# Performance work log

Measured on AMD Instinct MI355X. Metric: run time of the kernel, lower is better.

Reference implementation:

```python
import jax, jax.numpy as jnp
import numpy as np

E, H, V, KV, B, L = 512, 1024, 50257, 1000, 64, 512


def setup_inputs() -> dict:
    key = jax.random.key(0)
    ks = jax.random.split(key, 32)

    def p(i, shape, scale=0.02):
        return jax.random.normal(ks[i], shape, jnp.float32) * scale

    return {
        # forward args
        "input_ids": jax.random.randint(ks[0], (B,), 0, V),
        "h": p(1, (B, H), 1.0),
        "c": p(2, (B, H), 1.0),
        "k": p(3, (KV, E), 1.0),
        "context_vector": p(4, (B, H), 1.0),
        "encoder_outputs": p(5, (B, L, H), 1.0),
        # parameters (stored [in, out])
        "embedding": p(6, (V, E)),
        "W_ih": p(7, (E, 4 * H)),
        "W_hh": p(8, (H, 4 * H)),
        "b_ih": jnp.zeros((4 * H,), jnp.float32),
        "b_hh": jnp.zeros((4 * H,), jnp.float32),
        # attn MLP: Linear(2H,E) Tanh Linear(E,E) Tanh Linear(E,1)
        "aW1": p(9, (2 * H, E)), "ab1": jnp.zeros((E,), jnp.float32),
        "aW2": p(10, (E, E)), "ab2": jnp.zeros((E,), jnp.float32),
        "aW3": p(11, (E, 1)), "ab3": jnp.zeros((1,), jnp.float32),
        # attn_key MLP: Linear(E+2H,E) Tanh Linear(E,E) Tanh Linear(E,1)
        "kW1": p(12, (E + 2 * H, E)), "kb1": jnp.zeros((E,), jnp.float32),
        "kW2": p(13, (E, E)), "kb2": jnp.zeros((E,), jnp.float32),
        "kW3": p(14, (E, 1)), "kb3": jnp.zeros((1,), jnp.float32),
        # attn_linear: Linear(2H, V)
        "alW": p(15, (2 * H, V)), "alb": jnp.zeros((V,), jnp.float32),
    }


def reference(input_ids, h, c, k, context_vector, encoder_outputs,
              embedding, W_ih, W_hh, b_ih, b_hh,
              aW1, ab1, aW2, ab2, aW3, ab3,
              kW1, kb1, kW2, kb2, kW3, kb3,
              alW, alb):
    b = h.shape[0]
    kv = k.shape[0]
    v = alb.shape[0]

    # embedding lookup (dropout is identity in eval)
    x = embedding[input_ids]                                    # [B,E]

    # LSTMCell (PyTorch gate order: i, f, g, o)
    gates = x @ W_ih + h @ W_hh + b_ih + b_hh                   # [B,4H]
    i_g, f_g, g_g, o_g = jnp.split(gates, 4, axis=1)
    c_t = jax.nn.sigmoid(f_g) * c + jax.nn.sigmoid(i_g) * jnp.tanh(g_g)
    h_t = jax.nn.sigmoid(o_g) * jnp.tanh(c_t)                   # [B,H]

    # additive attention over encoder outputs
    h_ext = jnp.broadcast_to(h_t[:, None, :], encoder_outputs.shape)
    u = jnp.concatenate([encoder_outputs, h_ext], axis=2)       # [B,L,2H]
    u = jnp.tanh(u @ aW1 + ab1)
    u = jnp.tanh(u @ aW2 + ab2)
    u = (u @ aW3 + ab3)[..., 0]                                  # [B,L]
    a_t = jax.nn.softmax(u, axis=1)
    h_ctx = jnp.einsum('bl,blh->bh', a_t, encoder_outputs)       # [B,H]

    # key attention: cat(context, h_t, k) -> MLP -> [B,KV]
    ctx_ext = jnp.broadcast_to(context_vector[:, None, :], (b, kv, context_vector.shape[1]))
    ht_ext = jnp.broadcast_to(h_t[:, None, :], (b, kv, h_t.shape[1]))
    k_ext = jnp.broadcast_to(k[None, :, :], (b, kv, k.shape[1]))
    uk = jnp.concatenate([ctx_ext, ht_ext, k_ext], axis=2)       # [B,KV,E+2H]
    uk = jnp.tanh(uk @ kW1 + kb1)
    uk = jnp.tanh(uk @ kW2 + kb2)
    uk = (uk @ kW3 + kb3)[..., 0]                                # [B,KV]

    # zero-pad key logits into the full vocab (first V-KV entries are zero)
    v_k_t = jnp.concatenate([jnp.zeros((b, v - kv), h_t.dtype), uk], axis=1)

    # key_flag == 'True' path
    o_t = jnp.concatenate([h_t, h_ctx], axis=1) @ alW + alb + v_k_t  # [B,V]
    y_t = jax.nn.log_softmax(o_t, axis=1)
    return (y_t, h_t, c_t)
```

## Files before the change

### kernel.cpp

```cpp
#include <hip/hip_runtime.h>
#include <hip/hip_bf16.h>
#include <math.h>

#define EE 512
#define HH 1024
#define VV 50257
#define KVN 1000
#define BB 64
#define LL 512
#define FH 4096
#define TWOH 2048

typedef __hip_bfloat16 bf16;
typedef short bf16x8 __attribute__((ext_vector_type(8)));
typedef float f32x4  __attribute__((ext_vector_type(4)));

__device__ __forceinline__ float sigm(float x){ return 1.0f/(1.0f+__expf(-x)); }

__device__ __forceinline__ unsigned short f2bf(float f){
  unsigned int u = __float_as_uint(f);
  unsigned int r = (u + 0x7FFFu + ((u >> 16) & 1u)) >> 16;
  return (unsigned short)r;
}

__global__ __launch_bounds__(256)
void k_gates_init(const float* __restrict__ b_ih, const float* __restrict__ b_hh,
                  float* __restrict__ gates){
  int i = blockIdx.x*256 + threadIdx.x;
  int j = i & (FH-1);
  gates[i] = b_ih[j] + b_hh[j];
}

__global__ __launch_bounds__(256)
void k_embed_gates(const int* __restrict__ ids, const float* __restrict__ h,
                   const float* __restrict__ emb,
                   const float* __restrict__ W_ih, const float* __restrict__ W_hh,
                   float* __restrict__ gates){
  __shared__ float Xs[64][68];
  __shared__ float Ws[64][68];
  const int tid = threadIdx.x;
  const int nbase = blockIdx.x*64;
  const int kbase = blockIdx.y*64;
  {
    int b = tid >> 2;
    int kof = (tid & 3)*16;
    int id = ids[b];
    #pragma unroll
    for (int i=0;i<16;i++){
      int kg = kbase + kof + i;
      float v = (kg < EE) ? emb[(size_t)id*EE + kg] : h[(size_t)b*HH + (kg-EE)];
      Xs[kof+i][b] = v;
    }
  }
  {
    int n = tid & 63;
    int kr0 = tid >> 6;
    #pragma unroll
    for (int i=0;i<16;i++){
      int kr = kr0 + i*4;
      int kg = kbase + kr;
      float v = (kg < EE) ? W_ih[(size_t)kg*FH + nbase + n]
                          : W_hh[(size_t)(kg-EE)*FH + nbase + n];
      Ws[kr][n] = v;
    }
  }
  __syncthreads();
  const int tx = tid & 15, ty = tid >> 4;
  float acc[4][4] = {};
  for (int k=0;k<64;k++){
    float4 a4 = *(const float4*)(&Xs[k][ty*4]);
    float4 w4 = *(const float4*)(&Ws[k][tx*4]);
    float aa[4] = {a4.x,a4.y,a4.z,a4.w};
    float ww[4] = {w4.x,w4.y,w4.z,w4.w};
    #pragma unroll
    for (int i=0;i<4;i++)
      #pragma unroll
      for (int j=0;j<4;j++)
        acc[i][j] += aa[i]*ww[j];
  }
  #pragma unroll
  for (int i=0;i<4;i++){
    int b = ty*4 + i;
    #pragma unroll
    for (int j=0;j<4;j++)
      atomicAdd(&gates[(size_t)b*FH + nbase + tx*4 + j], acc[i][j]);
  }
}

__global__ __launch_bounds__(256)
void k_lstm(const float* __restrict__ gates, const float* __restrict__ c_in,
            float* __restrict__ hout, float* __restrict__ cout){
  int idx = blockIdx.x*256 + threadIdx.x;
  int b = idx >> 10, hh = idx & 1023;
  const float* g = gates + (size_t)b*FH;
  float ig = g[hh], fg = g[HH+hh], gg = g[2*HH+hh], og = g[3*HH+hh];
  float ct = sigm(fg)*c_in[idx] + sigm(ig)*tanhf(gg);
  float ht = sigm(og)*tanhf(ct);
  hout[idx] = ht;
  cout[idx] = ct;
}

__global__ __launch_bounds__(256)
void k_q1p1(const float* __restrict__ ht, const float* __restrict__ ctx,
            const float* __restrict__ aW1, const float* __restrict__ ab1,
            const float* __restrict__ kW1, const float* __restrict__ kb1,
            float* __restrict__ q1, float* __restrict__ p1){
  int e = blockIdx.x*256 + threadIdx.x;
  int b = blockIdx.y;
  float aq = 0.f, ap = 0.f;
  for (int k2 = 0; k2 < HH; ++k2){
    float hv = ht[(size_t)b*HH + k2];
    float cv = ctx[(size_t)b*HH + k2];
    aq += hv * aW1[(size_t)(HH+k2)*EE + e];
    ap += cv * kW1[(size_t)k2*EE + e];
    ap += hv * kW1[(size_t)(HH+k2)*EE + e];
  }
  q1[(size_t)b*EE + e] = aq + ab1[e];
  p1[(size_t)b*EE + e] = ap + kb1[e];
}

__global__ __launch_bounds__(256)
void k_p2(const float* __restrict__ kin, const float* __restrict__ kW1,
          float* __restrict__ p2){
  int e  = blockIdx.x*256 + threadIdx.x;
  int kv = blockIdx.y;
  float a = 0.f;
  for (int k2 = 0; k2 < EE; ++k2)
    a += kin[(size_t)kv*EE + k2] * kW1[(size_t)(TWOH+k2)*EE + e];
  p2[(size_t)kv*EE + e] = a;
}

__global__ __launch_bounds__(256)
void k_transpose_bf16(const float* __restrict__ W, bf16* __restrict__ Wt,
                      int K, int N){
  __shared__ float t[32][33];
  int k0 = blockIdx.y*32, n0 = blockIdx.x*32;
  int tx = threadIdx.x & 31, ty = threadIdx.x >> 5;
  #pragma unroll
  for (int i=0;i<4;i++){
    int kk = ty + i*8;
    t[kk][tx] = W[(size_t)(k0+kk)*N + n0 + tx];
  }
  __syncthreads();
  #pragma unroll
  for (int i=0;i<4;i++){
    int nn = ty + i*8;
    Wt[(size_t)(n0+nn)*K + k0 + tx] = __float2bfloat16(t[tx][nn]);
  }
}

__global__ __launch_bounds__(256)
void k_mfma_tanh_dot(const bf16* __restrict__ A, const bf16* __restrict__ Wt,
                     const float* __restrict__ bias, const float* __restrict__ w3,
                     float* __restrict__ logits){
  __shared__ short As[128*40];
  __shared__ short Bs[128*40];
  const int tid  = threadIdx.x;
  const int lane = tid & 63, wid = tid >> 6;
  const int wm = wid >> 1, wn = wid & 1;
  const int quad = lane >> 4, l16 = lane & 15;
  const int m0 = blockIdx.y*128, n0 = blockIdx.x*128;

  f32x4 acc[4][4] = {};
  for (int k0 = 0; k0 < 512; k0 += 32){
    #pragma unroll
    for (int it = 0; it < 2; ++it){
      int task = tid + it*256;
      int row = task >> 2, cg = task & 3;
      *(bf16x8*)(As + row*40 + cg*8) =
        *(const bf16x8*)((const short*)A + (size_t)(m0+row)*512 + k0 + cg*8);
      *(bf16x8*)(Bs + row*40 + cg*8) =
        *(const bf16x8*)((const short*)Wt + (size_t)(n0+row)*512 + k0 + cg*8);
    }
    __syncthreads();
    bf16x8 af[4], bfr[4];
    #pragma unroll
    for (int mt=0; mt<4; ++mt)
      af[mt] = *(const bf16x8*)(As + (wm*64 + mt*16 + l16)*40 + quad*8);
    #pragma unroll
    for (int nt=0; nt<4; ++nt)
      bfr[nt] = *(const bf16x8*)(Bs + (wn*64 + nt*16 + l16)*40 + quad*8);
    #pragma unroll
    for (int mt=0; mt<4; ++mt)
      #pragma unroll
      for (int nt=0; nt<4; ++nt)
        acc[mt][nt] = __builtin_amdgcn_mfma_f32_16x16x32_bf16(af[mt], bfr[nt], acc[mt][nt], 0, 0, 0);
    __syncthreads();
  }
  float bv[4], wv[4];
  #pragma unroll
  for (int nt=0; nt<4; ++nt){
    int n = n0 + wn*64 + nt*16 + l16;
    bv[nt] = bias[n]; wv[nt] = w3[n];
  }
  #pragma unroll
  for (int mt=0; mt<4; ++mt){
    #pragma unroll
    for (int r=0; r<4; ++r){
      float s = 0.f;
      #pragma unroll
      for (int nt=0; nt<4; ++nt)
        s += tanhf(acc[mt][nt][r] + bv[nt]) * wv[nt];
      #pragma unroll
      for (int off=8; off>=1; off>>=1) s += __shfl_xor(s, off, 16);
      if (l16 == 0){
        int row = wm*64 + mt*16 + quad*4 + r;
        atomicAdd(&logits[m0 + row], s);
      }
    }
  }
}

__global__ __launch_bounds__(256)
void k_mfma_key(const float* __restrict__ p1, const float* __restrict__ p2,
                const bf16* __restrict__ Wt,
                const float* __restrict__ bias, const float* __restrict__ w3,
                float* __restrict__ logits){
  __shared__ short As[128*40];
  __shared__ short Bs[128*40];
  const int tid  = threadIdx.x;
  const int lane = tid & 63, wid = tid >> 6;
  const int wm = wid >> 1, wn = wid & 1;
  const int quad = lane >> 4, l16 = lane & 15;
  const int m0 = blockIdx.y*128, n0 = blockIdx.x*128;

  f32x4 acc[4][4] = {};
  for (int k0 = 0; k0 < 512; k0 += 32){
    #pragma unroll
    for (int it = 0; it < 2; ++it){
      int grp = tid + it*256;
      int row = grp >> 2, cg = grp & 3;
      int r = m0 + row;
      int b = r / KVN;
      int kv = r - b*KVN;
      int e = k0 + cg*8;
      float4 a0 = *(const float4*)(p1 + (size_t)b*EE + e);
      float4 a1 = *(const float4*)(p1 + (size_t)b*EE + e + 4);
      float4 c0 = *(const float4*)(p2 + (size_t)kv*EE + e);
      float4 c1 = *(const float4*)(p2 + (size_t)kv*EE + e + 4);
      bf16x8 v;
      v[0]=(short)f2bf(tanhf(a0.x+c0.x)); v[1]=(short)f2bf(tanhf(a0.y+c0.y));
      v[2]=(short)f2bf(tanhf(a0.z+c0.z)); v[3]=(short)f2bf(tanhf(a0.w+c0.w));
      v[4]=(short)f2bf(tanhf(a1.x+c1.x)); v[5]=(short)f2bf(tanhf(a1.y+c1.y));
      v[6]=(short)f2bf(tanhf(a1.z+c1.z)); v[7]=(short)f2bf(tanhf(a1.w+c1.w));
      *(bf16x8*)(As + row*40 + cg*8) = v;
      *(bf16x8*)(Bs + row*40 + cg*8) =
        *(const bf16x8*)((const short*)Wt + (size_t)(n0+row)*512 + k0 + cg*8);
    }
    __syncthreads();
    bf16x8 af[4], bfr[4];
    #pragma unroll
    for (int mt=0; mt<4; ++mt)
      af[mt] = *(const bf16x8*)(As + (wm*64 + mt*16 + l16)*40 + quad*8);
    #pragma unroll
    for (int nt=0; nt<4; ++nt)
      bfr[nt] = *(const bf16x8*)(Bs + (wn*64 + nt*16 + l16)*40 + quad*8);
    #pragma unroll
    for (int mt=0; mt<4; ++mt)
      #pragma unroll
      for (int nt=0; nt<4; ++nt)
        acc[mt][nt] = __builtin_amdgcn_mfma_f32_16x16x32_bf16(af[mt], bfr[nt], acc[mt][nt], 0, 0, 0);
    __syncthreads();
  }
  float bv[4], wv[4];
  #pragma unroll
  for (int nt=0; nt<4; ++nt){
    int n = n0 + wn*64 + nt*16 + l16;
    bv[nt] = bias[n]; wv[nt] = w3[n];
  }
  #pragma unroll
  for (int mt=0; mt<4; ++mt){
    #pragma unroll
    for (int r=0; r<4; ++r){
      float s = 0.f;
      #pragma unroll
      for (int nt=0; nt<4; ++nt)
        s += tanhf(acc[mt][nt][r] + bv[nt]) * wv[nt];
      #pragma unroll
      for (int off=8; off>=1; off>>=1) s += __shfl_xor(s, off, 16);
      if (l16 == 0){
        int row = wm*64 + mt*16 + quad*4 + r;
        atomicAdd(&logits[m0 + row], s);
      }
    }
  }
}

__global__ __launch_bounds__(256)
void k_mfma_a1(const float* __restrict__ enc, const bf16* __restrict__ Wt,
               const float* __restrict__ q1, bf16* __restrict__ U1){
  __shared__ short As[128*40];
  __shared__ short Bs[128*40];
  const int tid  = threadIdx.x;
  const int lane = tid & 63, wid = tid >> 6;
  const int wm = wid >> 1, wn = wid & 1;
  const int quad = lane >> 4, l16 = lane & 15;
  const int m0 = blockIdx.y*128, n0 = blockIdx.x*128;

  f32x4 acc[4][4] = {};
  for (int k0 = 0; k0 < 1024; k0 += 32){
    #pragma unroll
    for (int it = 0; it < 4; ++it){
      int task = tid + it*256;
      int row = task >> 3, g = task & 7;
      float4 f = *(const float4*)(enc + (size_t)(m0+row)*1024 + k0 + g*4);
      uint2 pk;
      pk.x = (unsigned int)f2bf(f.x) | ((unsigned int)f2bf(f.y) << 16);
      pk.y = (unsigned int)f2bf(f.z) | ((unsigned int)f2bf(f.w) << 16);
      *(uint2*)(As + row*40 + g*4) = pk;
    }
    #pragma unroll
    for (int it = 0; it < 2; ++it){
      int task = tid + it*256;
      int row = task >> 2, cg = task & 3;
      *(bf16x8*)(Bs + row*40 + cg*8) =
        *(const bf16x8*)((const short*)Wt + (size_t)(n0+row)*1024 + k0 + cg*8);
    }
    __syncthreads();
    bf16x8 af[4], bfr[4];
    #pragma unroll
    for (int mt=0; mt<4; ++mt)
      af[mt] = *(const bf16x8*)(As + (wm*64 + mt*16 + l16)*40 + quad*8);
    #pragma unroll
    for (int nt=0; nt<4; ++nt)
      bfr[nt] = *(const bf16x8*)(Bs + (wn*64 + nt*16 + l16)*40 + quad*8);
    #pragma unroll
    for (int mt=0; mt<4; ++mt)
      #pragma unroll
      for (int nt=0; nt<4; ++nt)
        acc[mt][nt] = __builtin_amdgcn_mfma_f32_16x16x32_bf16(af[mt], bfr[nt], acc[mt][nt], 0, 0, 0);
    __syncthreads();
  }
  const int b = m0 >> 9;
  const float* q1r = q1 + (size_t)b*EE;
  #pragma unroll
  for (int mt=0; mt<4; ++mt){
    #pragma unroll
    for (int r=0; r<4; ++r){
      int m = m0 + wm*64 + mt*16 + quad*4 + r;
      #pragma unroll
      for (int nt=0; nt<4; ++nt){
        int n = n0 + wn*64 + nt*16 + l16;
        U1[(size_t)m*EE + n] = __float2bfloat16(tanhf(acc[mt][nt][r] + q1r[n]));
      }
    }
  }
}

__global__ __launch_bounds__(256)
void k_init_logits(float* __restrict__ ulog, float* __restrict__ uklog,
                   const float* __restrict__ ab3, const float* __restrict__ kb3){
  int i = blockIdx.x*256 + threadIdx.x;
  if (i < BB*LL)  ulog[i]  = ab3[0];
  if (i < BB*KVN) uklog[i] = kb3[0];
}

__global__ __launch_bounds__(256)
void k_softmax(float* __restrict__ ulog){
  __shared__ float sdata[256];
  int b = blockIdx.x, tid = threadIdx.x;
  float* row = ulog + (size_t)b*LL;
  float v0 = row[tid], v1 = row[tid+256];
  sdata[tid] = fmaxf(v0, v1);
  __syncthreads();
  for (int s=128;s>0;s>>=1){ if (tid<s) sdata[tid]=fmaxf(sdata[tid],sdata[tid+s]); __syncthreads(); }
  float mx = sdata[0];
  __syncthreads();
  float e0 = __expf(v0-mx), e1 = __expf(v1-mx);
  sdata[tid] = e0+e1;
  __syncthreads();
  for (int s=128;s>0;s>>=1){ if (tid<s) sdata[tid]+=sdata[tid+s]; __syncthreads(); }
  float inv = 1.f/sdata[0];
  row[tid]     = e0*inv;
  row[tid+256] = e1*inv;
}

__global__ __launch_bounds__(256)
void k_hctx(const float* __restrict__ a, const float* __restrict__ enc,
            float* __restrict__ hctx){
  int hh = blockIdx.x*256 + threadIdx.x;
  int b  = blockIdx.y;
  float s = 0.f;
  for (int l=0;l<LL;l++)
    s += a[(size_t)b*LL + l] * enc[((size_t)b*LL + l)*HH + hh];
  hctx[(size_t)b*HH + hh] = s;
}

__global__ __launch_bounds__(256)
void k_hcat_bf16(const float* __restrict__ ht, const float* __restrict__ hctx,
                 bf16* __restrict__ hcatb){
  int idx = blockIdx.x*256 + threadIdx.x;
  int b = idx >> 11, kk = idx & 2047;
  float v = (kk < HH) ? ht[(size_t)b*HH + kk] : hctx[(size_t)b*HH + (kk-HH)];
  hcatb[idx] = __float2bfloat16(v);
}

__global__ __launch_bounds__(256)
void k_y_init(const float* __restrict__ alb, const float* __restrict__ uklog,
              float* __restrict__ y){
  int idx = blockIdx.x*256 + threadIdx.x;
  if (idx >= BB*VV) return;
  int b = idx / VV;
  int v = idx - b*VV;
  float o = alb[v];
  int dk = v - (VV - KVN);
  if (dk >= 0) o += uklog[b*KVN + dk];
  y[idx] = o;
}

__global__ __launch_bounds__(256)
void k_final_mfma(const bf16* __restrict__ hcatb, const float* __restrict__ alW,
                  float* __restrict__ y){
  __shared__ short As[64*40];
  __shared__ float Bs[32*133];
  const int tid  = threadIdx.x;
  const int lane = tid & 63, wid = tid >> 6;
  const int quad = lane >> 4, l16 = lane & 15;
  const int n0 = blockIdx.x*128;
  const int kc0 = blockIdx.y*512;

  f32x4 acc[4][2] = {};
  for (int k0 = 0; k0 < 512; k0 += 32){
    {
      int row = tid >> 2, cg = tid & 3;
      *(bf16x8*)(As + row*40 + cg*8) =
        *(const bf16x8*)((const short*)hcatb + (size_t)row*TWOH + kc0 + k0 + cg*8);
    }
    #pragma unroll
    for (int i=0;i<16;i++){
      int flat = tid + i*256;
      int kk = flat >> 7, n = flat & 127;
      int gv = n0 + n;
      float v = (gv < VV) ? alW[(size_t)(kc0 + k0 + kk)*VV + gv] : 0.f;
      Bs[kk*133 + n] = v;
    }
    __syncthreads();
    bf16x8 af[4], bfr[2];
    #pragma unroll
    for (int mt=0; mt<4; ++mt)
      af[mt] = *(const bf16x8*)(As + (mt*16 + l16)*40 + quad*8);
    #pragma unroll
    for (int nt=0; nt<2; ++nt){
      int nloc = wid*32 + nt*16 + l16;
      bf16x8 v;
      #pragma unroll
      for (int j=0;j<8;j++)
        v[j] = (short)f2bf(Bs[(quad*8 + j)*133 + nloc]);
      bfr[nt] = v;
    }
    #pragma unroll
    for (int mt=0; mt<4; ++mt)
      #pragma unroll
      for (int nt=0; nt<2; ++nt)
        acc[mt][nt] = __builtin_amdgcn_mfma_f32_16x16x32_bf16(af[mt], bfr[nt], acc[mt][nt], 0, 0, 0);
    __syncthreads();
  }
  #pragma unroll
  for (int nt=0; nt<2; ++nt){
    int v = n0 + wid*32 + nt*16 + l16;
    if (v < VV){
      #pragma unroll
      for (int mt=0; mt<4; ++mt){
        #pragma unroll
        for (int r=0; r<4; ++r){
          int b = mt*16 + quad*4 + r;
          atomicAdd(&y[(size_t)b*VV + v], acc[mt][nt][r]);
        }
      }
    }
  }
}

#define LSE_CH 6283
__global__ __launch_bounds__(256)
void k_lse_part(const float* __restrict__ y, float* __restrict__ pmax,
                float* __restrict__ psum){
  __shared__ float sm[256], ss[256];
  int b = blockIdx.y, chunk = blockIdx.x, tid = threadIdx.x;
  int start = chunk*LSE_CH;
  int end = start + LSE_CH; if (end > VV) end = VV;
  const float* row = y + (size_t)b*VV;
  float m = -1e30f, s = 0.f;
  for (int i = start + tid; i < end; i += 256){
    float v = row[i];
    if (v > m){ s = s*__expf(m - v) + 1.f; m = v; }
    else s += __expf(v - m);
  }
  sm[tid] = m; ss[tid] = s;
  __syncthreads();
  for (int st=128; st>0; st>>=1){
    if (tid < st){
      float m2 = sm[tid+st], s2 = ss[tid+st];
      float M = fmaxf(sm[tid], m2);
      ss[tid] = ss[tid]*__expf(sm[tid]-M) + s2*__expf(m2-M);
      sm[tid] = M;
    }
    __syncthreads();
  }
  if (tid == 0){ pmax[b*8 + chunk] = sm[0]; psum[b*8 + chunk] = ss[0]; }
}

__global__ __launch_bounds__(64)
void k_lse_combine(const float* __restrict__ pmax, const float* __restrict__ psum,
                   float* __restrict__ lse){
  int b = threadIdx.x;
  float m = -1e30f;
  #pragma unroll
  for (int i=0;i<8;i++) m = fmaxf(m, pmax[b*8+i]);
  float s = 0.f;
  #pragma unroll
  for (int i=0;i<8;i++) s += psum[b*8+i]*__expf(pmax[b*8+i]-m);
  lse[b] = m + logf(s);
}

__global__ __launch_bounds__(256)
void k_lse_apply(float* __restrict__ y, const float* __restrict__ lse){
  int idx = blockIdx.x*256 + threadIdx.x;
  if (idx >= BB*VV) return;
  int b = idx / VV;
  y[idx] -= lse[b];
}

extern "C" void kernel_launch(void* const* d_in, const int* in_sizes, int n_in,
                              void* d_out, int out_size, void* d_ws, size_t ws_size,
                              hipStream_t stream) {
  const int*   ids  = (const int*)  d_in[0];
  const float* h    = (const float*)d_in[1];
  const float* c    = (const float*)d_in[2];
  const float* kin  = (const float*)d_in[3];
  const float* ctx  = (const float*)d_in[4];
  const float* enc  = (const float*)d_in[5];
  const float* emb  = (const float*)d_in[6];
  const float* W_ih = (const float*)d_in[7];
  const float* W_hh = (const float*)d_in[8];
  const float* b_ih = (const float*)d_in[9];
  const float* b_hh = (const float*)d_in[10];
  const float* aW1  = (const float*)d_in[11];
  const float* ab1  = (const float*)d_in[12];
  const float* aW2  = (const float*)d_in[13];
  const float* ab2  = (const float*)d_in[14];
  const float* aW3  = (const float*)d_in[15];
  const float* ab3  = (const float*)d_in[16];
  const float* kW1  = (const float*)d_in[17];
  const float* kb1  = (const float*)d_in[18];
  const float* kW2  = (const float*)d_in[19];
  const float* kb2  = (const float*)d_in[20];
  const float* kW3  = (const float*)d_in[21];
  const float* kb3  = (const float*)d_in[22];
  const float* alW  = (const float*)d_in[23];
  const float* alb  = (const float*)d_in[24];

  float* y      = (float*)d_out;
  float* ht_out = y + (size_t)BB*VV;
  float* ct_out = ht_out + (size_t)BB*HH;

  char* w = (char*)d_ws;
  float* gates = (float*)w;  w += (size_t)BB*FH*4;
  float* q1    = (float*)w;  w += (size_t)BB*EE*4;
  float* p1    = (float*)w;  w += (size_t)BB*EE*4;
  float* p2    = (float*)w;  w += (size_t)KVN*EE*4;
  float* ulog  = (float*)w;  w += (size_t)BB*LL*4;
  float* uklog = (float*)w;  w += (size_t)BB*KVN*4;
  float* hctx  = (float*)w;  w += (size_t)BB*HH*4;
  bf16*  hcatb = (bf16*)w;   w += (size_t)BB*TWOH*2;
  bf16*  U1    = (bf16*)w;   w += (size_t)BB*LL*EE*2;
  bf16*  aW1t  = (bf16*)w;   w += (size_t)EE*HH*2;
  bf16*  aW2t  = (bf16*)w;   w += (size_t)EE*EE*2;
  bf16*  kW2t  = (bf16*)w;   w += (size_t)EE*EE*2;
  float* pmax  = (float*)w;  w += (size_t)BB*8*4;
  float* psum  = (float*)w;  w += (size_t)BB*8*4;
  float* lse   = (float*)w;  w += (size_t)BB*4;

  const int NBLK = (BB*VV + 255)/256;

  k_transpose_bf16<<<dim3(EE/32, HH/32), 256, 0, stream>>>(aW1, aW1t, HH, EE);
  k_transpose_bf16<<<dim3(EE/32, EE/32), 256, 0, stream>>>(aW2, aW2t, EE, EE);
  k_transpose_bf16<<<dim3(EE/32, EE/32), 256, 0, stream>>>(kW2, kW2t, EE, EE);

  k_gates_init<<<(BB*FH)/256, 256, 0, stream>>>(b_ih, b_hh, gates);
  k_embed_gates<<<dim3(FH/64, (EE+HH)/64), 256, 0, stream>>>(ids, h, emb, W_ih, W_hh, gates);
  k_lstm<<<(BB*HH)/256, 256, 0, stream>>>(gates, c, ht_out, ct_out);

  k_init_logits<<<(BB*KVN)/256 + 1, 256, 0, stream>>>(ulog, uklog, ab3, kb3);

  k_q1p1<<<dim3(EE/256, BB), 256, 0, stream>>>(ht_out, ctx, aW1, ab1, kW1, kb1, q1, p1);
  k_p2<<<dim3(EE/256, KVN), 256, 0, stream>>>(kin, kW1, p2);

  k_mfma_key<<<dim3(4, (BB*KVN)/128), 256, 0, stream>>>(p1, p2, kW2t, kb2, kW3, uklog);

  k_mfma_a1<<<dim3(4, (BB*LL)/128), 256, 0, stream>>>(enc, aW1t, q1, U1);
  k_mfma_tanh_dot<<<dim3(4, (BB*LL)/128), 256, 0, stream>>>(U1, aW2t, ab2, aW3, ulog);
  k_softmax<<<BB, 256, 0, stream>>>(ulog);
  k_hctx<<<dim3(HH/256, BB), 256, 0, stream>>>(ulog, enc, hctx);

  k_hcat_bf16<<<(BB*TWOH)/256, 256, 0, stream>>>(ht_out, hctx, hcatb);
  k_y_init<<<NBLK, 256, 0, stream>>>(alb, uklog, y);
  k_final_mfma<<<dim3((VV+127)/128, 4), 256, 0, stream>>>(hcatb, alW, y);
  k_lse_part<<<dim3(8, BB), 256, 0, stream>>>(y, pmax, psum);
  k_lse_combine<<<1, 64, 0, stream>>>(pmax, psum, lse);
  k_lse_apply<<<NBLK, 256, 0, stream>>>(y, lse);
}
```

Measured before the change: 1.458 ms.

## Retile MFMA kernels to full-N blocks, fuse softmax/hctx/epilogues, drop atomics

The three MFMA MLP kernels now have each block cover 32 rows against the full 512 output columns, so the tanh-dot reduction is finished in shared memory and written directly instead of with atomicAdd. The separate logit-init kernel therefore goes away. The attention softmax is fused into the context kernel, which writes bf16 into the concat buffer; h_t is written there by the LSTM kernel. The final vocabulary GEMM no longer splits K, so the bias and key logits are added in its epilogue and the y-init and atomic passes are removed. The LSE combine step is folded into the apply kernel. Fewer launches and atomics come at the cost of smaller per-block tiles, a larger B-tile load per block, and uncoalesced alW reads.

```diff
diff --git a/kernel.cpp b/kernel.cpp
--- a/kernel.cpp
+++ b/kernel.cpp
@@ -89,7 +89,8 @@
 
 __global__ __launch_bounds__(256)
 void k_lstm(const float* __restrict__ gates, const float* __restrict__ c_in,
-            float* __restrict__ hout, float* __restrict__ cout){
+            float* __restrict__ hout, float* __restrict__ cout,
+            bf16* __restrict__ hcatb){
   int idx = blockIdx.x*256 + threadIdx.x;
   int b = idx >> 10, hh = idx & 1023;
   const float* g = gates + (size_t)b*FH;
@@ -98,6 +99,7 @@
   float ht = sigm(og)*tanhf(ct);
   hout[idx] = ht;
   cout[idx] = ct;
+  hcatb[(size_t)b*TWOH + hh] = __float2bfloat16(ht);
 }
 
 __global__ __launch_bounds__(256)
@@ -149,65 +151,71 @@
   }
 }
 
+
 __global__ __launch_bounds__(256)
 void k_mfma_tanh_dot(const bf16* __restrict__ A, const bf16* __restrict__ Wt,
                      const float* __restrict__ bias, const float* __restrict__ w3,
-                     float* __restrict__ logits){
-  __shared__ short As[128*40];
-  __shared__ short Bs[128*40];
+                     const float* __restrict__ b3, float* __restrict__ logits){
+  __shared__ short As[32*40];
+  __shared__ short Bs[512*40];
+  __shared__ float red[4][32];
   const int tid  = threadIdx.x;
   const int lane = tid & 63, wid = tid >> 6;
-  const int wm = wid >> 1, wn = wid & 1;
   const int quad = lane >> 4, l16 = lane & 15;
-  const int m0 = blockIdx.y*128, n0 = blockIdx.x*128;
-
-  f32x4 acc[4][4] = {};
+  const int m0 = blockIdx.x*32;
+
+  f32x4 acc[2][8] = {};
   for (int k0 = 0; k0 < 512; k0 += 32){
-    #pragma unroll
-    for (int it = 0; it < 2; ++it){
-      int task = tid + it*256;
-      int row = task >> 2, cg = task & 3;
+    if (tid < 128){
+      int row = tid >> 2, cg = tid & 3;
       *(bf16x8*)(As + row*40 + cg*8) =
         *(const bf16x8*)((const short*)A + (size_t)(m0+row)*512 + k0 + cg*8);
+    }
+    #pragma unroll
+    for (int it = 0; it < 8; ++it){
+      int grp = tid + it*256;
+      int row = grp >> 2, cg = grp & 3;
       *(bf16x8*)(Bs + row*40 + cg*8) =
-        *(const bf16x8*)((const short*)Wt + (size_t)(n0+row)*512 + k0 + cg*8);
-    }
-    __syncthreads();
-    bf16x8 af[4], bfr[4];
-    #pragma unroll
-    for (int mt=0; mt<4; ++mt)
-      af[mt] = *(const bf16x8*)(As + (wm*64 + mt*16 + l16)*40 + quad*8);
-    #pragma unroll
-    for (int nt=0; nt<4; ++nt)
-      bfr[nt] = *(const bf16x8*)(Bs + (wn*64 + nt*16 + l16)*40 + quad*8);
-    #pragma unroll
-    for (int mt=0; mt<4; ++mt)
-      #pragma unroll
-      for (int nt=0; nt<4; ++nt)
+        *(const bf16x8*)((const short*)Wt + (size_t)row*512 + k0 + cg*8);
+    }
+    __syncthreads();
+    bf16x8 af[2], bfr[8];
+    #pragma unroll
+    for (int mt=0; mt<2; ++mt)
+      af[mt] = *(const bf16x8*)(As + (mt*16 + l16)*40 + quad*8);
+    #pragma unroll
+    for (int nt=0; nt<8; ++nt)
+      bfr[nt] = *(const bf16x8*)(Bs + (wid*128 + nt*16 + l16)*40 + quad*8);
+    #pragma unroll
+    for (int mt=0; mt<2; ++mt)
+      #pragma unroll
+      for (int nt=0; nt<8; ++nt)
         acc[mt][nt] = __builtin_amdgcn_mfma_f32_16x16x32_bf16(af[mt], bfr[nt], acc[mt][nt], 0, 0, 0);
     __syncthreads();
   }
-  float bv[4], wv[4];
-  #pragma unroll
-  for (int nt=0; nt<4; ++nt){
-    int n = n0 + wn*64 + nt*16 + l16;
+  float bv[8], wv[8];
+  #pragma unroll
+  for (int nt=0; nt<8; ++nt){
+    int n = wid*128 + nt*16 + l16;
     bv[nt] = bias[n]; wv[nt] = w3[n];
   }
   #pragma unroll
-  for (int mt=0; mt<4; ++mt){
+  for (int mt=0; mt<2; ++mt){
     #pragma unroll
     for (int r=0; r<4; ++r){
       float s = 0.f;
       #pragma unroll
-      for (int nt=0; nt<4; ++nt)
+      for (int nt=0; nt<8; ++nt)
         s += tanhf(acc[mt][nt][r] + bv[nt]) * wv[nt];
       #pragma unroll
       for (int off=8; off>=1; off>>=1) s += __shfl_xor(s, off, 16);
-      if (l16 == 0){
-        int row = wm*64 + mt*16 + quad*4 + r;
-        atomicAdd(&logits[m0 + row], s);
-      }
-    }
+      if (l16 == 0) red[wid][mt*16 + quad*4 + r] = s;
+    }
+  }
+  __syncthreads();
+  if (tid < 32){
+    float s = red[0][tid] + red[1][tid] + red[2][tid] + red[3][tid];
+    logits[m0 + tid] = s + b3[0];
   }
 }
 
@@ -215,94 +223,92 @@
 void k_mfma_key(const float* __restrict__ p1, const float* __restrict__ p2,
                 const bf16* __restrict__ Wt,
                 const float* __restrict__ bias, const float* __restrict__ w3,
-                float* __restrict__ logits){
-  __shared__ short As[128*40];
-  __shared__ short Bs[128*40];
+                const float* __restrict__ b3, float* __restrict__ logits){
+  __shared__ short As[32*40];
+  __shared__ short Bs[512*40];
+  __shared__ float red[4][32];
   const int tid  = threadIdx.x;
   const int lane = tid & 63, wid = tid >> 6;
-  const int wm = wid >> 1, wn = wid & 1;
   const int quad = lane >> 4, l16 = lane & 15;
-  const int m0 = blockIdx.y*128, n0 = blockIdx.x*128;
-
-  f32x4 acc[4][4] = {};
+  const int m0 = blockIdx.x*32;
+
+  f32x4 acc[2][8] = {};
   for (int k0 = 0; k0 < 512; k0 += 32){
-    #pragma unroll
-    for (int it = 0; it < 2; ++it){
+    {
+      int row = tid >> 3, g = tid & 7;
+      int m = m0 + row;
+      int b = m / KVN;
+      int kv = m - b*KVN;
+      int e = k0 + g*4;
+      float4 a0 = *(const float4*)(p1 + (size_t)b*EE + e);
+      float4 c0 = *(const float4*)(p2 + (size_t)kv*EE + e);
+      uint2 pk;
+      pk.x = (unsigned int)f2bf(tanhf(a0.x+c0.x)) | ((unsigned int)f2bf(tanhf(a0.y+c0.y)) << 16);
+      pk.y = (unsigned int)f2bf(tanhf(a0.z+c0.z)) | ((unsigned int)f2bf(tanhf(a0.w+c0.w)) << 16);
+      *(uint2*)(As + row*40 + g*4) = pk;
+    }
+    #pragma unroll
+    for (int it = 0; it < 8; ++it){
       int grp = tid + it*256;
       int row = grp >> 2, cg = grp & 3;
-      int r = m0 + row;
-      int b = r / KVN;
-      int kv = r - b*KVN;
-      int e = k0 + cg*8;
-      float4 a0 = *(const float4*)(p1 + (size_t)b*EE + e);
-      float4 a1 = *(const float4*)(p1 + (size_t)b*EE + e + 4);
-      float4 c0 = *(const float4*)(p2 + (size_t)kv*EE + e);
-      float4 c1 = *(const float4*)(p2 + (size_t)kv*EE + e + 4);
-      bf16x8 v;
-      v[0]=(short)f2bf(tanhf(a0.x+c0.x)); v[1]=(short)f2bf(tanhf(a0.y+c0.y));
-      v[2]=(short)f2bf(tanhf(a0.z+c0.z)); v[3]=(short)f2bf(tanhf(a0.w+c0.w));
-      v[4]=(short)f2bf(tanhf(a1.x+c1.x)); v[5]=(short)f2bf(tanhf(a1.y+c1.y));
-      v[6]=(short)f2bf(tanhf(a1.z+c1.z)); v[7]=(short)f2bf(tanhf(a1.w+c1.w));
-      *(bf16x8*)(As + row*40 + cg*8) = v;
       *(bf16x8*)(Bs + row*40 + cg*8) =
-        *(const bf16x8*)((const short*)Wt + (size_t)(n0+row)*512 + k0 + cg*8);
-    }
-    __syncthreads();
-    bf16x8 af[4], bfr[4];
-    #pragma unroll
-    for (int mt=0; mt<4; ++mt)
-      af[mt] = *(const bf16x8*)(As + (wm*64 + mt*16 + l16)*40 + quad*8);
-    #pragma unroll
-    for (int nt=0; nt<4; ++nt)
-      bfr[nt] = *(const bf16x8*)(Bs + (wn*64 + nt*16 + l16)*40 + quad*8);
-    #pragma unroll
-    for (int mt=0; mt<4; ++mt)
-      #pragma unroll
-      for (int nt=0; nt<4; ++nt)
+        *(const bf16x8*)((const short*)Wt + (size_t)row*512 + k0 + cg*8);
+    }
+    __syncthreads();
+    bf16x8 af[2], bfr[8];
+    #pragma unroll
+    for (int mt=0; mt<2; ++mt)
+      af[mt] = *(const bf16x8*)(As + (mt*16 + l16)*40 + quad*8);
+    #pragma unroll
+    for (int nt=0; nt<8; ++nt)
+      bfr[nt] = *(const bf16x8*)(Bs + (wid*128 + nt*16 + l16)*40 + quad*8);
+    #pragma unroll
+    for (int mt=0; mt<2; ++mt)
+      #pragma unroll
+      for (int nt=0; nt<8; ++nt)
         acc[mt][nt] = __builtin_amdgcn_mfma_f32_16x16x32_bf16(af[mt], bfr[nt], acc[mt][nt], 0, 0, 0);
     __syncthreads();
   }
-  float bv[4], wv[4];
-  #pragma unroll
-  for (int nt=0; nt<4; ++nt){
-    int n = n0 + wn*64 + nt*16 + l16;
+  float bv[8], wv[8];
+  #pragma unroll
+  for (int nt=0; nt<8; ++nt){
+    int n = wid*128 + nt*16 + l16;
     bv[nt] = bias[n]; wv[nt] = w3[n];
   }
   #pragma unroll
-  for (int mt=0; mt<4; ++mt){
+  for (int mt=0; mt<2; ++mt){
     #pragma unroll
     for (int r=0; r<4; ++r){
       float s = 0.f;
       #pragma unroll
-      for (int nt=0; nt<4; ++nt)
+      for (int nt=0; nt<8; ++nt)
         s += tanhf(acc[mt][nt][r] + bv[nt]) * wv[nt];
       #pragma unroll
       for (int off=8; off>=1; off>>=1) s += __shfl_xor(s, off, 16);
-      if (l16 == 0){
-        int row = wm*64 + mt*16 + quad*4 + r;
-        atomicAdd(&logits[m0 + row], s);
-      }
-    }
+      if (l16 == 0) red[wid][mt*16 + quad*4 + r] = s;
+    }
+  }
+  __syncthreads();
+  if (tid < 32){
+    float s = red[0][tid] + red[1][tid] + red[2][tid] + red[3][tid];
+    logits[m0 + tid] = s + b3[0];
   }
 }
 
 __global__ __launch_bounds__(256)
 void k_mfma_a1(const float* __restrict__ enc, const bf16* __restrict__ Wt,
                const float* __restrict__ q1, bf16* __restrict__ U1){
-  __shared__ short As[128*40];
-  __shared__ short Bs[128*40];
+  __shared__ short As[32*40];
+  __shared__ short Bs[512*40];
   const int tid  = threadIdx.x;
   const int lane = tid & 63, wid = tid >> 6;
-  const int wm = wid >> 1, wn = wid & 1;
   const int quad = lane >> 4, l16 = lane & 15;
-  const int m0 = blockIdx.y*128, n0 = blockIdx.x*128;
-
-  f32x4 acc[4][4] = {};
+  const int m0 = blockIdx.x*32;
+
+  f32x4 acc[2][8] = {};
   for (int k0 = 0; k0 < 1024; k0 += 32){
-    #pragma unroll
-    for (int it = 0; it < 4; ++it){
-      int task = tid + it*256;
-      int row = task >> 3, g = task & 7;
+    {
+      int row = tid >> 3, g = tid & 7;
       float4 f = *(const float4*)(enc + (size_t)(m0+row)*1024 + k0 + g*4);
       uint2 pk;
       pk.x = (unsigned int)f2bf(f.x) | ((unsigned int)f2bf(f.y) << 16);
@@ -310,37 +316,37 @@
       *(uint2*)(As + row*40 + g*4) = pk;
     }
     #pragma unroll
-    for (int it = 0; it < 2; ++it){
-      int task = tid + it*256;
-      int row = task >> 2, cg = task & 3;
+    for (int it = 0; it < 8; ++it){
+      int grp = tid + it*256;
+      int row = grp >> 2, cg = grp & 3;
       *(bf16x8*)(Bs + row*40 + cg*8) =
-        *(const bf16x8*)((const short*)Wt + (size_t)(n0+row)*1024 + k0 + cg*8);
-    }
-    __syncthreads();
-    bf16x8 af[4], bfr[4];
-    #pragma unroll
-    for (int mt=0; mt<4; ++mt)
-      af[mt] = *(const bf16x8*)(As + (wm*64 + mt*16 + l16)*40 + quad*8);
-    #pragma unroll
-    for (int nt=0; nt<4; ++nt)
-      bfr[nt] = *(const bf16x8*)(Bs + (wn*64 + nt*16 + l16)*40 + quad*8);
-    #pragma unroll
-    for (int mt=0; mt<4; ++mt)
-      #pragma unroll
-      for (int nt=0; nt<4; ++nt)
+        *(const bf16x8*)((const short*)Wt + (size_t)row*1024 + k0 + cg*8);
+    }
+    __syncthreads();
+    bf16x8 af[2], bfr[8];
+    #pragma unroll
+    for (int mt=0; mt<2; ++mt)
+      af[mt] = *(const bf16x8*)(As + (mt*16 + l16)*40 + quad*8);
+    #pragma unroll
+    for (int nt=0; nt<8; ++nt)
+      bfr[nt] = *(const bf16x8*)(Bs + (wid*128 + nt*16 + l16)*40 + quad*8);
+    #pragma unroll
+    for (int mt=0; mt<2; ++mt)
+      #pragma unroll
+      for (int nt=0; nt<8; ++nt)
         acc[mt][nt] = __builtin_amdgcn_mfma_f32_16x16x32_bf16(af[mt], bfr[nt], acc[mt][nt], 0, 0, 0);
     __syncthreads();
   }
   const int b = m0 >> 9;
   const float* q1r = q1 + (size_t)b*EE;
   #pragma unroll
-  for (int mt=0; mt<4; ++mt){
+  for (int mt=0; mt<2; ++mt){
     #pragma unroll
     for (int r=0; r<4; ++r){
-      int m = m0 + wm*64 + mt*16 + quad*4 + r;
-      #pragma unroll
-      for (int nt=0; nt<4; ++nt){
-        int n = n0 + wn*64 + nt*16 + l16;
+      int m = m0 + mt*16 + quad*4 + r;
+      #pragma unroll
+      for (int nt=0; nt<8; ++nt){
+        int n = wid*128 + nt*16 + l16;
         U1[(size_t)m*EE + n] = __float2bfloat16(tanhf(acc[mt][nt][r] + q1r[n]));
       }
     }
@@ -348,124 +354,83 @@
 }
 
 __global__ __launch_bounds__(256)
-void k_init_logits(float* __restrict__ ulog, float* __restrict__ uklog,
-                   const float* __restrict__ ab3, const float* __restrict__ kb3){
-  int i = blockIdx.x*256 + threadIdx.x;
-  if (i < BB*LL)  ulog[i]  = ab3[0];
-  if (i < BB*KVN) uklog[i] = kb3[0];
-}
-
-__global__ __launch_bounds__(256)
-void k_softmax(float* __restrict__ ulog){
-  __shared__ float sdata[256];
-  int b = blockIdx.x, tid = threadIdx.x;
-  float* row = ulog + (size_t)b*LL;
-  float v0 = row[tid], v1 = row[tid+256];
-  sdata[tid] = fmaxf(v0, v1);
-  __syncthreads();
-  for (int s=128;s>0;s>>=1){ if (tid<s) sdata[tid]=fmaxf(sdata[tid],sdata[tid+s]); __syncthreads(); }
-  float mx = sdata[0];
-  __syncthreads();
-  float e0 = __expf(v0-mx), e1 = __expf(v1-mx);
-  sdata[tid] = e0+e1;
-  __syncthreads();
-  for (int s=128;s>0;s>>=1){ if (tid<s) sdata[tid]+=sdata[tid+s]; __syncthreads(); }
-  float inv = 1.f/sdata[0];
-  row[tid]     = e0*inv;
-  row[tid+256] = e1*inv;
-}
-
-__global__ __launch_bounds__(256)
-void k_hctx(const float* __restrict__ a, const float* __restrict__ enc,
-            float* __restrict__ hctx){
-  int hh = blockIdx.x*256 + threadIdx.x;
-  int b  = blockIdx.y;
+void k_hctx(const float* __restrict__ ulog, const float* __restrict__ enc,
+            bf16* __restrict__ hcatb){
+  __shared__ float wts[512];
+  __shared__ float red[256];
+  int b = blockIdx.y, tid = threadIdx.x;
+  const float* row = ulog + (size_t)b*LL;
+  float u0 = row[tid], u1 = row[tid+256];
+  red[tid] = fmaxf(u0, u1);
+  __syncthreads();
+  for (int s=128;s>0;s>>=1){ if (tid<s) red[tid]=fmaxf(red[tid],red[tid+s]); __syncthreads(); }
+  float mx = red[0];
+  __syncthreads();
+  float e0 = __expf(u0-mx), e1 = __expf(u1-mx);
+  red[tid] = e0+e1;
+  __syncthreads();
+  for (int s=128;s>0;s>>=1){ if (tid<s) red[tid]+=red[tid+s]; __syncthreads(); }
+  float inv = 1.f/red[0];
+  wts[tid] = e0*inv; wts[tid+256] = e1*inv;
+  __syncthreads();
+  int hh = blockIdx.x*256 + tid;
   float s = 0.f;
   for (int l=0;l<LL;l++)
-    s += a[(size_t)b*LL + l] * enc[((size_t)b*LL + l)*HH + hh];
-  hctx[(size_t)b*HH + hh] = s;
-}
-
-__global__ __launch_bounds__(256)
-void k_hcat_bf16(const float* __restrict__ ht, const float* __restrict__ hctx,
-                 bf16* __restrict__ hcatb){
-  int idx = blockIdx.x*256 + threadIdx.x;
-  int b = idx >> 11, kk = idx & 2047;
-  float v = (kk < HH) ? ht[(size_t)b*HH + kk] : hctx[(size_t)b*HH + (kk-HH)];
-  hcatb[idx] = __float2bfloat16(v);
-}
-
-__global__ __launch_bounds__(256)
-void k_y_init(const float* __restrict__ alb, const float* __restrict__ uklog,
-              float* __restrict__ y){
-  int idx = blockIdx.x*256 + threadIdx.x;
-  if (idx >= BB*VV) return;
-  int b = idx / VV;
-  int v = idx - b*VV;
-  float o = alb[v];
-  int dk = v - (VV - KVN);
-  if (dk >= 0) o += uklog[b*KVN + dk];
-  y[idx] = o;
+    s += wts[l] * enc[((size_t)b*LL + l)*HH + hh];
+  hcatb[(size_t)b*TWOH + HH + hh] = __float2bfloat16(s);
 }
 
 __global__ __launch_bounds__(256)
 void k_final_mfma(const bf16* __restrict__ hcatb, const float* __restrict__ alW,
+                  const float* __restrict__ alb, const float* __restrict__ uklog,
                   float* __restrict__ y){
   __shared__ short As[64*40];
-  __shared__ float Bs[32*133];
+  __shared__ short Bs[64*40];
   const int tid  = threadIdx.x;
   const int lane = tid & 63, wid = tid >> 6;
   const int quad = lane >> 4, l16 = lane & 15;
-  const int n0 = blockIdx.x*128;
-  const int kc0 = blockIdx.y*512;
-
-  f32x4 acc[4][2] = {};
-  for (int k0 = 0; k0 < 512; k0 += 32){
+  const int n0 = blockIdx.x*64;
+
+  f32x4 acc[4] = {};
+  const int nst = tid & 63;
+  const int kst = (tid >> 6)*8;
+  const int vst = n0 + nst;
+  const bool okst = vst < VV;
+  for (int k0 = 0; k0 < TWOH; k0 += 32){
     {
-      int row = tid >> 2, cg = tid & 3;
-      *(bf16x8*)(As + row*40 + cg*8) =
-        *(const bf16x8*)((const short*)hcatb + (size_t)row*TWOH + kc0 + k0 + cg*8);
-    }
-    #pragma unroll
-    for (int i=0;i<16;i++){
-      int flat = tid + i*256;
-      int kk = flat >> 7, n = flat & 127;
-      int gv = n0 + n;
-      float v = (gv < VV) ? alW[(size_t)(kc0 + k0 + kk)*VV + gv] : 0.f;
-      Bs[kk*133 + n] = v;
-    }
-    __syncthreads();
-    bf16x8 af[4], bfr[2];
-    #pragma unroll
-    for (int mt=0; mt<4; ++mt)
-      af[mt] = *(const bf16x8*)(As + (mt*16 + l16)*40 + quad*8);
-    #pragma unroll
-    for (int nt=0; nt<2; ++nt){
-      int nloc = wid*32 + nt*16 + l16;
-      bf16x8 v;
-      #pragma unroll
-      for (int j=0;j<8;j++)
-        v[j] = (short)f2bf(Bs[(quad*8 + j)*133 + nloc]);
-      bfr[nt] = v;
-    }
-    #pragma unroll
-    for (int mt=0; mt<4; ++mt)
-      #pragma unroll
-      for (int nt=0; nt<2; ++nt)
-        acc[mt][nt] = __builtin_amdgcn_mfma_f32_16x16x32_bf16(af[mt], bfr[nt], acc[mt][nt], 0, 0, 0);
-    __syncthreads();
-  }
-  #pragma unroll
-  for (int nt=0; nt<2; ++nt){
-    int v = n0 + wid*32 + nt*16 + l16;
-    if (v < VV){
-      #pragma unroll
-      for (int mt=0; mt<4; ++mt){
-        #pragma unroll
-        for (int r=0; r<4; ++r){
-          int b = mt*16 + quad*4 + r;
-          atomicAdd(&y[(size_t)b*VV + v], acc[mt][nt][r]);
-        }
+      int rowm = tid >> 2, cg = tid & 3;
+      *(bf16x8*)(As + rowm*40 + cg*8) =
+        *(const bf16x8*)((const short*)hcatb + (size_t)rowm*TWOH + k0 + cg*8);
+    }
+    {
+      #pragma unroll
+      for (int j=0;j<8;j++){
+        int kk = kst + j;
+        float v = okst ? alW[(size_t)(k0+kk)*VV + vst] : 0.f;
+        Bs[nst*40 + kk] = (short)f2bf(v);
+      }
+    }
+    __syncthreads();
+    bf16x8 bfr = *(const bf16x8*)(Bs + (wid*16 + l16)*40 + quad*8);
+    #pragma unroll
+    for (int mt=0; mt<4; ++mt){
+      bf16x8 af = *(const bf16x8*)(As + (mt*16 + l16)*40 + quad*8);
+      acc[mt] = __builtin_amdgcn_mfma_f32_16x16x32_bf16(af, bfr, acc[mt], 0, 0, 0);
+    }
+    __syncthreads();
+  }
+  int v = n0 + wid*16 + l16;
+  if (v < VV){
+    float bias = alb[v];
+    int dk = v - (VV - KVN);
+    #pragma unroll
+    for (int mt=0; mt<4; ++mt){
+      #pragma unroll
+      for (int r=0; r<4; ++r){
+        int b = mt*16 + quad*4 + r;
+        float o = acc[mt][r] + bias;
+        if (dk >= 0) o += uklog[b*KVN + dk];
+        y[(size_t)b*VV + v] = o;
       }
     }
   }
@@ -500,25 +465,19 @@
   if (tid == 0){ pmax[b*8 + chunk] = sm[0]; psum[b*8 + chunk] = ss[0]; }
 }
 
-__global__ __launch_bounds__(64)
-void k_lse_combine(const float* __restrict__ pmax, const float* __restrict__ psum,
-                   float* __restrict__ lse){
-  int b = threadIdx.x;
-  float m = -1e30f;
-  #pragma unroll
-  for (int i=0;i<8;i++) m = fmaxf(m, pmax[b*8+i]);
-  float s = 0.f;
-  #pragma unroll
-  for (int i=0;i<8;i++) s += psum[b*8+i]*__expf(pmax[b*8+i]-m);
-  lse[b] = m + logf(s);
-}
-
-__global__ __launch_bounds__(256)
-void k_lse_apply(float* __restrict__ y, const float* __restrict__ lse){
+__global__ __launch_bounds__(256)
+void k_lse_apply(float* __restrict__ y, const float* __restrict__ pmax,
+                 const float* __restrict__ psum){
   int idx = blockIdx.x*256 + threadIdx.x;
   if (idx >= BB*VV) return;
   int b = idx / VV;
-  y[idx] -= lse[b];
+  float m = -1e30f;
+  #pragma unroll
+  for (int i=0;i<8;i++) m = fmaxf(m, pmax[b*8+i]);
+  float s = 0.f;
+  #pragma unroll
+  for (int i=0;i<8;i++) s += psum[b*8+i]*__expf(pmax[b*8+i]-m);
+  y[idx] -= m + logf(s);
 }
 
 extern "C" void kernel_launch(void* const* d_in, const int* in_sizes, int n_in,
@@ -561,7 +520,6 @@
   float* p2    = (float*)w;  w += (size_t)KVN*EE*4;
   float* ulog  = (float*)w;  w += (size_t)BB*LL*4;
   float* uklog = (float*)w;  w += (size_t)BB*KVN*4;
-  float* hctx  = (float*)w;  w += (size_t)BB*HH*4;
   bf16*  hcatb = (bf16*)w;   w += (size_t)BB*TWOH*2;
   bf16*  U1    = (bf16*)w;   w += (size_t)BB*LL*EE*2;
   bf16*  aW1t  = (bf16*)w;   w += (size_t)EE*HH*2;
@@ -569,7 +527,6 @@
   bf16*  kW2t  = (bf16*)w;   w += (size_t)EE*EE*2;
   float* pmax  = (float*)w;  w += (size_t)BB*8*4;
   float* psum  = (float*)w;  w += (size_t)BB*8*4;
-  float* lse   = (float*)w;  w += (size_t)BB*4;
 
   const int NBLK = (BB*VV + 255)/256;
 
@@ -579,24 +536,18 @@
 
   k_gates_init<<<(BB*FH)/256, 256, 0, stream>>>(b_ih, b_hh, gates);
   k_embed_gates<<<dim3(FH/64, (EE+HH)/64), 256, 0, stream>>>(ids, h, emb, W_ih, W_hh, gates);
-  k_lstm<<<(BB*HH)/256, 256, 0, stream>>>(gates, c, ht_out, ct_out);
-
-  k_init_logits<<<(BB*KVN)/256 + 1, 256, 0, stream>>>(ulog, uklog, ab3, kb3);
+  k_lstm<<<(BB*HH)/256, 256, 0, stream>>>(gates, c, ht_out, ct_out, hcatb);
 
   k_q1p1<<<dim3(EE/256, BB), 256, 0, stream>>>(ht_out, ctx, aW1, ab1, kW1, kb1, q1, p1);
   k_p2<<<dim3(EE/256, KVN), 256, 0, stream>>>(kin, kW1, p2);
 
-  k_mfma_key<<<dim3(4, (BB*KVN)/128), 256, 0, stream>>>(p1, p2, kW2t, kb2, kW3, uklog);
-
-  k_mfma_a1<<<dim3(4, (BB*LL)/128), 256, 0, stream>>>(enc, aW1t, q1, U1);
-  k_mfma_tanh_dot<<<dim3(4, (BB*LL)/128), 256, 0, stream>>>(U1, aW2t, ab2, aW3, ulog);
-  k_softmax<<<BB, 256, 0, stream>>>(ulog);
-  k_hctx<<<dim3(HH/256, BB), 256, 0, stream>>>(ulog, enc, hctx);
-
-  k_hcat_bf16<<<(BB*TWOH)/256, 256, 0, stream>>>(ht_out, hctx, hcatb);
-  k_y_init<<<NBLK, 256, 0, stream>>>(alb, uklog, y);
-  k_final_mfma<<<dim3((VV+127)/128, 4), 256, 0, stream>>>(hcatb, alW, y);
+  k_mfma_key<<<(BB*KVN)/32, 256, 0, stream>>>(p1, p2, kW2t, kb2, kW3, kb3, uklog);
+
+  k_mfma_a1<<<(BB*LL)/32, 256, 0, stream>>>(enc, aW1t, q1, U1);
+  k_mfma_tanh_dot<<<(BB*LL)/32, 256, 0, stream>>>(U1, aW2t, ab2, aW3, ab3, ulog);
+  k_hctx<<<dim3(HH/256, BB), 256, 0, stream>>>(ulog, enc, hcatb);
+
+  k_final_mfma<<<(VV + 63)/64, 256, 0, stream>>>(hcatb, alW, alb, uklog, y);
   k_lse_part<<<dim3(8, BB), 256, 0, stream>>>(y, pmax, psum);
-  k_lse_combine<<<1, 64, 0, stream>>>(pmax, psum, lse);
-  k_lse_apply<<<NBLK, 256, 0, stream>>>(y, lse);
-}
+  k_lse_apply<<<NBLK, 256, 0, stream>>>(y, pmax, psum);
+}
```

After: 1.498 ms. 2.7% more time.
